# Kernel optimization log

Hardware: AMD Instinct MI355X
Metric: run time of the kernel (lower is better)

## Reference

```python
import jax, jax.numpy as jnp
import numpy as np

B, H, DH = 1, 16, 128
HID, MLP = 2048, 8192
LT, LI = 256, 2048
L = LT + LI


def _layernorm(x, eps=1e-6):
    mu = jnp.mean(x, axis=-1, keepdims=True)
    var = jnp.mean((x - mu) ** 2, axis=-1, keepdims=True)
    return (x - mu) * jax.lax.rsqrt(var + eps)


def _rmsnorm(x, scale, eps=1e-6):
    rr = jax.lax.rsqrt(jnp.mean(x * x, axis=-1, keepdims=True) + eps)
    return x * rr * scale


def _apply_rope(x, pe):
    # x: (B,H,L,D) -> (B,H,L,D/2,1,2); pe: (B,1,L,D/2,2,2)
    xs = x.reshape(*x.shape[:-1], -1, 1, 2)
    out = pe[..., 0] * xs[..., 0] + pe[..., 1] * xs[..., 1]  # (B,H,L,D/2,2)
    return out.reshape(x.shape)


def _qkv_split(x, w, b):
    Bv, Lv, _ = x.shape
    qkv = (x @ w + b).reshape(Bv, Lv, 3, H, DH).transpose(2, 0, 3, 1, 4)  # K B H L D
    return qkv[0], qkv[1], qkv[2]


def setup_inputs() -> dict:
    key = jax.random.key(0)
    ks = jax.random.split(key, 16)
    s = 0.02
    inp = {
        'img': jax.random.normal(ks[0], (B, LI, HID), jnp.float32),
        'txt': jax.random.normal(ks[1], (B, LT, HID), jnp.float32),
        'vec': jax.random.normal(ks[2], (B, HID), jnp.float32),
        'img_mod_w': s * jax.random.normal(ks[3], (HID, 6 * HID), jnp.float32),
        'img_mod_b': jnp.zeros((6 * HID,), jnp.float32),
        'txt_mod_w': s * jax.random.normal(ks[4], (HID, 6 * HID), jnp.float32),
        'txt_mod_b': jnp.zeros((6 * HID,), jnp.float32),
        'img_qkv_w': s * jax.random.normal(ks[5], (HID, 3 * HID), jnp.float32),
        'img_qkv_b': jnp.zeros((3 * HID,), jnp.float32),
        'img_q_scale': jnp.ones((DH,), jnp.float32),
        'img_k_scale': jnp.ones((DH,), jnp.float32),
        'txt_qkv_w': s * jax.random.normal(ks[6], (HID, 3 * HID), jnp.float32),
        'txt_qkv_b': jnp.zeros((3 * HID,), jnp.float32),
        'txt_q_scale': jnp.ones((DH,), jnp.float32),
        'txt_k_scale': jnp.ones((DH,), jnp.float32),
        'img_proj_w': s * jax.random.normal(ks[7], (HID, HID), jnp.float32),
        'img_proj_b': jnp.zeros((HID,), jnp.float32),
        'txt_proj_w': s * jax.random.normal(ks[8], (HID, HID), jnp.float32),
        'txt_proj_b': jnp.zeros((HID,), jnp.float32),
        'img_mlp_w1': s * jax.random.normal(ks[9], (HID, MLP), jnp.float32),
        'img_mlp_b1': jnp.zeros((MLP,), jnp.float32),
        'img_mlp_w2': s * jax.random.normal(ks[10], (MLP, HID), jnp.float32),
        'img_mlp_b2': jnp.zeros((HID,), jnp.float32),
        'txt_mlp_w1': s * jax.random.normal(ks[11], (HID, MLP), jnp.float32),
        'txt_mlp_b1': jnp.zeros((MLP,), jnp.float32),
        'txt_mlp_w2': s * jax.random.normal(ks[12], (MLP, HID), jnp.float32),
        'txt_mlp_b2': jnp.zeros((HID,), jnp.float32),
    }
    # Real RoPE rotation matrices [[cos,-sin],[sin,cos]]: (1,1,L,DH/2,2,2)
    pos = jnp.arange(L, dtype=jnp.float32)
    freqs = 1.0 / (10000.0 ** (jnp.arange(DH // 2, dtype=jnp.float32) / (DH // 2)))
    ang = pos[:, None] * freqs[None, :]
    c, sn = jnp.cos(ang), jnp.sin(ang)
    pe = jnp.stack([jnp.stack([c, -sn], -1), jnp.stack([sn, c], -1)], -2)  # (L,DH/2,2,2)
    inp['pe'] = pe[None, None]
    return inp


def reference(img, txt, vec, pe,
              img_mod_w, img_mod_b, txt_mod_w, txt_mod_b,
              img_qkv_w, img_qkv_b, img_q_scale, img_k_scale,
              txt_qkv_w, txt_qkv_b, txt_q_scale, txt_k_scale,
              img_proj_w, img_proj_b, txt_proj_w, txt_proj_b,
              img_mlp_w1, img_mlp_b1, img_mlp_w2, img_mlp_b2,
              txt_mlp_w1, txt_mlp_b1, txt_mlp_w2, txt_mlp_b2):
    # AdaLN modulation: SiLU(vec) @ W -> 6 chunks of (B,1,HID)
    im = jnp.split(jax.nn.silu(vec) @ img_mod_w + img_mod_b, 6, axis=-1)
    i_sh1, i_sc1, i_g1, i_sh2, i_sc2, i_g2 = [m[:, None, :] for m in im]
    tm = jnp.split(jax.nn.silu(vec) @ txt_mod_w + txt_mod_b, 6, axis=-1)
    t_sh1, t_sc1, t_g1, t_sh2, t_sc2, t_g2 = [m[:, None, :] for m in tm]

    img_mod = (1 + i_sc1) * _layernorm(img) + i_sh1
    iq, ik, iv = _qkv_split(img_mod, img_qkv_w, img_qkv_b)
    iq = _rmsnorm(iq, img_q_scale)
    ik = _rmsnorm(ik, img_k_scale)

    txt_mod = (1 + t_sc1) * _layernorm(txt) + t_sh1
    tq, tk, tv = _qkv_split(txt_mod, txt_qkv_w, txt_qkv_b)
    tq = _rmsnorm(tq, txt_q_scale)
    tk = _rmsnorm(tk, txt_k_scale)

    # concat text then image along sequence (B,H,L,D)
    q = jnp.concatenate([tq, iq], axis=2)
    k = jnp.concatenate([tk, ik], axis=2)
    v = jnp.concatenate([tv, iv], axis=2)
    q = _apply_rope(q, pe)
    k = _apply_rope(k, pe)

    scores = jnp.einsum('bhqd,bhkd->bhqk', q, k) / np.float32(np.sqrt(DH))
    a = jax.nn.softmax(scores, axis=-1)
    o = jnp.einsum('bhqk,bhkd->bhqd', a, v)
    attn = o.transpose(0, 2, 1, 3).reshape(o.shape[0], -1, H * DH)  # (B,L,HID)

    txt_a, img_a = attn[:, :LT], attn[:, LT:]

    img = img + i_g1 * (img_a @ img_proj_w + img_proj_b)
    h = (1 + i_sc2) * _layernorm(img) + i_sh2
    h = jax.nn.gelu(h @ img_mlp_w1 + img_mlp_b1, approximate=True)
    img = img + i_g2 * (h @ img_mlp_w2 + img_mlp_b2)

    txt = txt + t_g1 * (txt_a @ txt_proj_w + txt_proj_b)
    h = (1 + t_sc2) * _layernorm(txt) + t_sh2
    h = jax.nn.gelu(h @ txt_mlp_w1 + txt_mlp_b1, approximate=True)
    txt = txt + t_g2 * (h @ txt_mlp_w2 + txt_mlp_b2)

    return img, txt
```

## Files before the change

kernel.cpp:

```cpp
#include <hip/hip_runtime.h>

using u16 = unsigned short;
typedef __bf16 bf16x8 __attribute__((ext_vector_type(8)));
typedef float f32x4 __attribute__((ext_vector_type(4)));

__device__ inline u16 f2bf(float f){
  unsigned u = __float_as_uint(f);
  u += 0x7fff + ((u >> 16) & 1);
  return (u16)(u >> 16);
}

__device__ inline float wredsum(float v){
  #pragma unroll
  for (int o = 32; o; o >>= 1) v += __shfl_xor(v, o, 64);
  return v;
}

__device__ inline void gld16(const u16* g, u16* lds){
  __builtin_amdgcn_global_load_lds(
      (const __attribute__((address_space(1))) unsigned int*)g,
      (__attribute__((address_space(3))) unsigned int*)lds, 16, 0, 0);
}

__global__ void mod_matvec_k(const float* __restrict__ vec,
    const float* __restrict__ wi, const float* __restrict__ bi,
    const float* __restrict__ wt, const float* __restrict__ bt,
    float* __restrict__ oi, float* __restrict__ ot)
{
  __shared__ float sv[2048];
  __shared__ float red[4][64];
  int tid = threadIdx.x;
  for (int i = tid; i < 2048; i += 256){ float v = vec[i]; sv[i] = v / (1.0f + __expf(-v)); }
  __syncthreads();
  int j0 = blockIdx.x * 64;
  bool ist = j0 >= 12288;
  const float* w = ist ? wt : wi;
  const float* b = ist ? bt : bi;
  float* o = ist ? ot : oi;
  int col = (ist ? j0 - 12288 : j0) + (tid & 63);
  int kq = tid >> 6;
  float acc = 0.f;
  const float* wp = w + col;
  for (int k = kq * 512; k < kq * 512 + 512; ++k) acc += sv[k] * wp[(long long)k * 12288];
  red[kq][tid & 63] = acc;
  __syncthreads();
  if (kq == 0){
    o[col] = red[0][tid] + red[1][tid] + red[2][tid] + red[3][tid] + b[col];
  }
}

struct TcArgs {
  const float* in[8];
  u16* out[8];
  int K[8];
  int N[8];
  int base[9];
};

__global__ void tcast8_k(TcArgs a)
{
  __shared__ float tile[32][33];
  int bid = blockIdx.x;
  int w = 0;
  #pragma unroll
  for (int i = 0; i < 8; ++i) if (bid >= a.base[i + 1]) w = i + 1;
  const float* in = a.in[w];
  u16* out = a.out[w];
  int K = a.K[w], N = a.N[w];
  int local = bid - a.base[w];
  int tx = N >> 5;
  int n0 = (local % tx) * 32, k0 = (local / tx) * 32;
  int tid = threadIdx.x;
  int r = tid >> 3, c4 = (tid & 7) * 4;
  float4 v = *(const float4*)&in[(long long)(k0 + r) * N + n0 + c4];
  tile[r][c4 + 0] = v.x; tile[r][c4 + 1] = v.y; tile[r][c4 + 2] = v.z; tile[r][c4 + 3] = v.w;
  __syncthreads();
  int n = tid >> 3, kq = (tid & 7) * 4;
  ushort4 o;
  o.x = f2bf(tile[kq + 0][n]);
  o.y = f2bf(tile[kq + 1][n]);
  o.z = f2bf(tile[kq + 2][n]);
  o.w = f2bf(tile[kq + 3][n]);
  *(ushort4*)&out[(long long)(n0 + n) * K + k0 + kq] = o;
}

__global__ void ln_mod_k(const float* __restrict__ x,
    const float* __restrict__ sh, const float* __restrict__ sc,
    u16* __restrict__ out)
{
  int row = blockIdx.x, tid = threadIdx.x;
  const float* xr = x + (long long)row * 2048;
  float v[8]; float s = 0.f, s2 = 0.f;
  #pragma unroll
  for (int j = 0; j < 8; ++j){ v[j] = xr[tid + j * 256]; s += v[j]; s2 += v[j] * v[j]; }
  s = wredsum(s); s2 = wredsum(s2);
  __shared__ float red[4][2];
  int wave = tid >> 6, lane = tid & 63;
  if (lane == 0){ red[wave][0] = s; red[wave][1] = s2; }
  __syncthreads();
  float S1 = red[0][0] + red[1][0] + red[2][0] + red[3][0];
  float S2 = red[0][1] + red[1][1] + red[2][1] + red[3][1];
  float mu = S1 * (1.0f / 2048.0f);
  float var = S2 * (1.0f / 2048.0f) - mu * mu;
  float rs = rsqrtf(var + 1e-6f);
  u16* orow = out + (long long)row * 2048;
  #pragma unroll
  for (int j = 0; j < 8; ++j){
    int c = tid + j * 256;
    orow[c] = f2bf((1.0f + sc[c]) * (v[j] - mu) * rs + sh[c]);
  }
}

__global__ void qkv_post_k(const float* __restrict__ qkv, int pos0,
    const float* __restrict__ qs, const float* __restrict__ ks,
    const float* __restrict__ pe,
    u16* __restrict__ Q, u16* __restrict__ Ko, u16* __restrict__ Vt)
{
  __shared__ u16 vs[128][72];
  int h = blockIdx.y;
  int t0 = blockIdx.x * 64;
  int tid = threadIdx.x, wave = tid >> 6, lane = tid & 63;
  for (int it = 0; it < 16; ++it){
    int tl = it * 4 + wave;
    int t = t0 + tl;
    const float* rp = qkv + (long long)t * 6144 + h * 128;
    float q0 = rp[lane],        q1 = rp[lane + 64];
    float k0 = rp[2048 + lane], k1 = rp[2048 + lane + 64];
    float v0 = rp[4096 + lane], v1 = rp[4096 + lane + 64];
    float qss = wredsum(q0 * q0 + q1 * q1);
    float kss = wredsum(k0 * k0 + k1 * k1);
    float rq = rsqrtf(qss * (1.0f / 128.0f) + 1e-6f) * 0.08838834764831845f;
    float rk = rsqrtf(kss * (1.0f / 128.0f) + 1e-6f);
    float qn0 = q0 * rq * qs[lane], qn1 = q1 * rq * qs[lane + 64];
    float kn0 = k0 * rk * ks[lane], kn1 = k1 * rk * ks[lane + 64];
    int pos = pos0 + t;
    const float* peb = pe + (long long)pos * 256;
    bool odd = lane & 1;
    float4 p0 = *(const float4*)&peb[(lane >> 1) * 4];
    float4 p1 = *(const float4*)&peb[128 + (lane >> 1) * 4];
    float c00 = odd ? p0.z : p0.x, c01 = odd ? p0.w : p0.y;
    float c10 = odd ? p1.z : p1.x, c11 = odd ? p1.w : p1.y;
    float qp0 = __shfl_xor(qn0, 1, 64), qp1 = __shfl_xor(qn1, 1, 64);
    float kp0 = __shfl_xor(kn0, 1, 64), kp1 = __shfl_xor(kn1, 1, 64);
    float qe0 = odd ? qp0 : qn0, qo0 = odd ? qn0 : qp0;
    float qe1 = odd ? qp1 : qn1, qo1 = odd ? qn1 : qp1;
    float ke0 = odd ? kp0 : kn0, ko0 = odd ? kn0 : kp0;
    float ke1 = odd ? kp1 : kn1, ko1 = odd ? kn1 : kp1;
    u16* Qr = Q  + ((long long)h * 2304 + pos) * 128;
    u16* Kr = Ko + ((long long)h * 2304 + pos) * 128;
    Qr[lane]      = f2bf(c00 * qe0 + c01 * qo0);
    Qr[lane + 64] = f2bf(c10 * qe1 + c11 * qo1);
    Kr[lane]      = f2bf(c00 * ke0 + c01 * ko0);
    Kr[lane + 64] = f2bf(c10 * ke1 + c11 * ko1);
    vs[lane][tl]      = f2bf(v0);
    vs[lane + 64][tl] = f2bf(v1);
  }
  __syncthreads();
  int dd = tid >> 1, co = (tid & 1) * 32;
  u16* vr = Vt + ((long long)h * 128 + dd) * 2304 + pos0 + t0 + co;
  #pragma unroll
  for (int u = 0; u < 8; ++u)
    *(ushort4*)(vr + u * 4) = *(const ushort4*)&vs[dd][co + u * 4];
}

__global__ __launch_bounds__(512)
void fattn_k(const u16* __restrict__ Qb, const u16* __restrict__ Kb,
             const u16* __restrict__ Vt, u16* __restrict__ attn)
{
  __shared__ u16 Pl[128 * 128];
  __shared__ u16 Kl[128 * 128];
  __shared__ u16 Vl[2][128 * 128];

  const int tid  = threadIdx.x;
  const int lane = tid & 63;
  const int wave = tid >> 6;
  const int h  = blockIdx.y;
  const int q0 = blockIdx.x * 128;

  const u16* Qg = Qb + ((long long)h * 2304 + q0) * 128;
  const u16* Kg = Kb + (long long)h * 2304 * 128;
  const u16* Vg = Vt + (long long)h * 128 * 2304;

  const int s_r   = wave * 4 + (lane >> 4);
  const int s_oct = lane & 15;
  auto stage = [&](const u16* g, int ldg, u16* lds){
    #pragma unroll
    for (int i = 0; i < 4; ++i){
      int row = i * 32 + s_r;
      gld16(g + (long long)row * ldg + ((s_oct ^ (row & 7)) * 8),
            lds + (i * 32 + wave * 4) * 128);
    }
  };

  stage(Qg, 128, Pl);
  stage(Kg, 128, Kl);
  stage(Vg, 2304, Vl[0]);
  __syncthreads();

  const int frow = lane & 15;
  const int j0   = lane >> 4;
  const int qrow = wave * 16 + frow;
  bf16x8 aq[4];
  #pragma unroll
  for (int s = 0; s < 4; ++s)
    aq[s] = *(const bf16x8*)&Pl[qrow * 128 + (((s * 4 + j0) ^ (qrow & 7)) * 8)];
  __syncthreads();

  float mrun[4], lrun[4];
  #pragma unroll
  for (int j = 0; j < 4; ++j){ mrun[j] = -3.0e38f; lrun[j] = 0.f; }
  f32x4 oacc[8] = {};

  for (int t = 0; t < 18; ++t){
    asm volatile("s_waitcnt vmcnt(0)" ::: "memory");
    __builtin_amdgcn_sched_barrier(0);
    __builtin_amdgcn_s_barrier();
    __builtin_amdgcn_sched_barrier(0);

    f32x4 sacc[8] = {};
    #pragma unroll
    for (int s = 0; s < 4; ++s){
      #pragma unroll
      for (int n = 0; n < 8; ++n){
        int kr = n * 16 + frow;
        bf16x8 bk = *(const bf16x8*)&Kl[kr * 128 + (((s * 4 + j0) ^ (kr & 7)) * 8)];
        sacc[n] = __builtin_amdgcn_mfma_f32_16x16x32_bf16(aq[s], bk, sacc[n], 0, 0, 0);
      }
    }
    __builtin_amdgcn_sched_barrier(0);
    __builtin_amdgcn_s_barrier();
    __builtin_amdgcn_sched_barrier(0);
    if (t + 1 < 18){
      stage(Kg + (long long)(t + 1) * 128 * 128, 128, Kl);
      stage(Vg + (t + 1) * 128, 2304, Vl[(t + 1) & 1]);
    }
    __builtin_amdgcn_sched_barrier(0);

    float mnew[4], scl[4];
    #pragma unroll
    for (int j = 0; j < 4; ++j){
      float v = sacc[0][j];
      #pragma unroll
      for (int n = 1; n < 8; ++n) v = fmaxf(v, sacc[n][j]);
      #pragma unroll
      for (int o = 8; o; o >>= 1) v = fmaxf(v, __shfl_xor(v, o, 64));
      mnew[j] = fmaxf(mrun[j], v);
      scl[j] = __expf(mrun[j] - mnew[j]);
      mrun[j] = mnew[j];
    }
    #pragma unroll
    for (int j = 0; j < 4; ++j){
      const int row = wave * 16 + j0 * 4 + j;
      float rsum = 0.f;
      #pragma unroll
      for (int n = 0; n < 8; ++n){
        float p = __expf(sacc[n][j] - mnew[j]);
        rsum += p;
        int col = n * 16 + frow;
        Pl[row * 128 + (((col >> 3) ^ (row & 7)) << 3) + (col & 7)] = f2bf(p);
      }
      #pragma unroll
      for (int o = 8; o; o >>= 1) rsum += __shfl_xor(rsum, o, 64);
      lrun[j] = lrun[j] * scl[j] + rsum;
      #pragma unroll
      for (int n = 0; n < 8; ++n) oacc[n][j] *= scl[j];
    }
    asm volatile("s_waitcnt lgkmcnt(0)" ::: "memory");
    __builtin_amdgcn_sched_barrier(0);

    const u16* vl = Vl[t & 1];
    #pragma unroll
    for (int s = 0; s < 4; ++s){
      bf16x8 ap = *(const bf16x8*)&Pl[qrow * 128 + (((s * 4 + j0) ^ (qrow & 7)) * 8)];
      #pragma unroll
      for (int n = 0; n < 8; ++n){
        int dr = n * 16 + frow;
        bf16x8 bv = *(const bf16x8*)&vl[dr * 128 + (((s * 4 + j0) ^ (dr & 7)) * 8)];
        oacc[n] = __builtin_amdgcn_mfma_f32_16x16x32_bf16(ap, bv, oacc[n], 0, 0, 0);
      }
    }
    __builtin_amdgcn_sched_barrier(0);
  }

  float inv[4];
  #pragma unroll
  for (int j = 0; j < 4; ++j) inv[j] = 1.0f / lrun[j];
  #pragma unroll
  for (int n = 0; n < 8; ++n){
    int d = n * 16 + frow;
    #pragma unroll
    for (int j = 0; j < 4; ++j){
      int row = wave * 16 + j0 * 4 + j;
      attn[(long long)(q0 + row) * 2048 + h * 128 + d] = f2bf(oacc[n][j] * inv[j]);
    }
  }
}

template<int MODE>
__global__ __launch_bounds__(512)
void gemm8_k(const u16* __restrict__ Ai, const u16* __restrict__ At, int lda,
             const u16* __restrict__ Bi, const u16* __restrict__ Bt, int ldb,
             const float* __restrict__ bias_i, const float* __restrict__ bias_t,
             const float* __restrict__ res_i,  const float* __restrict__ res_t,
             const float* __restrict__ gate_i, const float* __restrict__ gate_t,
             void* __restrict__ Ci, void* __restrict__ Ct, int ldc, int K)
{
  constexpr int BK = 64;
  constexpr int MR = 4, NR = 2;
  constexpr int AI = 2, BI = 2;

  __shared__ u16 As[2][128 * BK];
  __shared__ u16 Bs[2][128 * BK];

  const int tid  = threadIdx.x;
  const int lane = tid & 63;
  const int wave = tid >> 6;
  const int wm = wave >> 2;
  const int wn = wave & 3;

  const int gx = gridDim.x;
  const int nwg = gx * gridDim.y;
  const int n = blockIdx.x + gx * blockIdx.y;
  const int s_id = (n & 7) * (nwg >> 3) + (n >> 3);
  const int bx = s_id % gx;
  const int by = s_id / gx;

  const bool ist = bx >= 16;
  const int rb = ist ? bx - 16 : bx;
  const u16* Ab = (ist ? At : Ai) + (long long)rb * 128 * lda;
  const u16* Bb = (ist ? Bt : Bi) + (long long)by * 128 * ldb;
  const float* bias = ist ? bias_t : bias_i;
  const float* res  = ist ? res_t  : res_i;
  const float* gate = ist ? gate_t : gate_i;
  void* C = ist ? Ct : Ci;

  const int srow = wave * 8 + (lane >> 3);
  const int sgo  = ((lane & 7) ^ ((lane >> 3) & 7)) * 8;
  const u16* agp[AI]; const u16* bgp[BI];
  int alo[AI], blo[BI];
  #pragma unroll
  for (int i = 0; i < AI; ++i){
    agp[i] = Ab + (long long)(i * 64 + srow) * lda + sgo;
    alo[i] = (i * 64 + wave * 8) * BK;
  }
  #pragma unroll
  for (int i = 0; i < BI; ++i){
    bgp[i] = Bb + (long long)(i * 64 + srow) * ldb + sgo;
    blo[i] = (i * 64 + wave * 8) * BK;
  }

  const int arow0 = wm * 64;
  const int frow  = lane & 15;
  const int fx    = lane & 7;
  const int j0    = lane >> 4;

  f32x4 acc[MR][NR] = {};

  #pragma unroll
  for (int i = 0; i < AI; ++i) gld16(agp[i], &As[0][alo[i]]);
  #pragma unroll
  for (int i = 0; i < BI; ++i) gld16(bgp[i], &Bs[0][blo[i]]);
  __builtin_amdgcn_sched_barrier(0);

  const int nt = K / BK;
  for (int t = 0; t < nt; ++t){
    if (t + 1 < nt){
      int k0 = (t + 1) * BK;
      int nb = (t + 1) & 1;
      #pragma unroll
      for (int i = 0; i < AI; ++i) gld16(agp[i] + k0, &As[nb][alo[i]]);
      #pragma unroll
      for (int i = 0; i < BI; ++i) gld16(bgp[i] + k0, &Bs[nb][blo[i]]);
      __builtin_amdgcn_sched_barrier(0);
      asm volatile("s_waitcnt vmcnt(4)" ::: "memory");
    } else {
      asm volatile("s_waitcnt vmcnt(0)" ::: "memory");
    }
    __builtin_amdgcn_sched_barrier(0);
    __builtin_amdgcn_s_barrier();
    __builtin_amdgcn_sched_barrier(0);

    const u16* as = As[t & 1];
    const u16* bs = Bs[t & 1];
    #pragma unroll
    for (int s = 0; s < 2; ++s){
      const int oct = (s * 4 + j0) ^ fx;
      bf16x8 bfr[NR];
      #pragma unroll
      for (int nn = 0; nn < NR; ++nn)
        bfr[nn] = *(const bf16x8*)&bs[(wn * 32 + nn * 16 + frow) * BK + oct * 8];
      __builtin_amdgcn_s_setprio(1);
      #pragma unroll
      for (int m = 0; m < MR; ++m){
        bf16x8 af = *(const bf16x8*)&as[(arow0 + m * 16 + frow) * BK + oct * 8];
        #pragma unroll
        for (int nn = 0; nn < NR; ++nn)
          acc[m][nn] = __builtin_amdgcn_mfma_f32_16x16x32_bf16(af, bfr[nn], acc[m][nn], 0, 0, 0);
      }
      __builtin_amdgcn_s_setprio(0);
    }
    __builtin_amdgcn_sched_barrier(0);
    __builtin_amdgcn_s_barrier();
    __builtin_amdgcn_sched_barrier(0);
  }

  const int lr = (lane >> 4) * 4;
  const int lc = lane & 15;
  const long long rowb = (long long)rb * 128 + arow0;
  const long long colb = (long long)by * 128 + wn * 32;
  #pragma unroll
  for (int mi = 0; mi < MR; ++mi){
    #pragma unroll
    for (int ni = 0; ni < NR; ++ni){
      long long col = colb + ni * 16 + lc;
      float bv = bias ? bias[col] : 0.0f;
      #pragma unroll
      for (int j = 0; j < 4; ++j){
        long long row = rowb + mi * 16 + lr + j;
        float v = acc[mi][ni][j] + bv;
        long long ci = row * (long long)ldc + col;
        if constexpr (MODE == 0) ((float*)C)[ci] = v;
        else if constexpr (MODE == 2) ((float*)C)[ci] = res[ci] + gate[col] * v;
        else {
          float z2 = 1.5957691216057308f * (v + 0.044715f * v * v * v);
          ((u16*)C)[ci] = f2bf(v / (1.0f + __expf(-z2)));
        }
      }
    }
  }
}

extern "C" void kernel_launch(void* const* d_in, const int* in_sizes, int n_in,
                              void* d_out, int out_size, void* d_ws, size_t ws_size,
                              hipStream_t stream)
{
  const float* img        = (const float*)d_in[0];
  const float* txt        = (const float*)d_in[1];
  const float* vec        = (const float*)d_in[2];
  const float* img_mod_w  = (const float*)d_in[3];
  const float* img_mod_b  = (const float*)d_in[4];
  const float* txt_mod_w  = (const float*)d_in[5];
  const float* txt_mod_b  = (const float*)d_in[6];
  const float* img_qkv_w  = (const float*)d_in[7];
  const float* img_qkv_b  = (const float*)d_in[8];
  const float* img_q_s    = (const float*)d_in[9];
  const float* img_k_s    = (const float*)d_in[10];
  const float* txt_qkv_w  = (const float*)d_in[11];
  const float* txt_qkv_b  = (const float*)d_in[12];
  const float* txt_q_s    = (const float*)d_in[13];
  const float* txt_k_s    = (const float*)d_in[14];
  const float* img_proj_w = (const float*)d_in[15];
  const float* img_proj_b = (const float*)d_in[16];
  const float* txt_proj_w = (const float*)d_in[17];
  const float* txt_proj_b = (const float*)d_in[18];
  const float* img_mlp_w1 = (const float*)d_in[19];
  const float* img_mlp_b1 = (const float*)d_in[20];
  const float* img_mlp_w2 = (const float*)d_in[21];
  const float* img_mlp_b2 = (const float*)d_in[22];
  const float* txt_mlp_w1 = (const float*)d_in[23];
  const float* txt_mlp_b1 = (const float*)d_in[24];
  const float* txt_mlp_w2 = (const float*)d_in[25];
  const float* txt_mlp_b2 = (const float*)d_in[26];
  const float* pe         = (const float*)d_in[27];

  char* ws = (char*)d_ws;
  size_t off = 0;
  auto alloc = [&](size_t b){ void* p = ws + off; off = (off + b + 255) & ~(size_t)255; return p; };

  u16* wq_i = (u16*)alloc(6144ll * 2048 * 2);
  u16* wq_t = (u16*)alloc(6144ll * 2048 * 2);
  u16* wp_i = (u16*)alloc(2048ll * 2048 * 2);
  u16* wp_t = (u16*)alloc(2048ll * 2048 * 2);
  u16* w1_i = (u16*)alloc(8192ll * 2048 * 2);
  u16* w1_t = (u16*)alloc(8192ll * 2048 * 2);
  u16* w2_i = (u16*)alloc(2048ll * 8192 * 2);
  u16* w2_t = (u16*)alloc(2048ll * 8192 * 2);
  float* mod_i = (float*)alloc(12288 * 4);
  float* mod_t = (float*)alloc(12288 * 4);
  u16* Qb   = (u16*)alloc(16ll * 2304 * 128 * 2);
  u16* Kb   = (u16*)alloc(16ll * 2304 * 128 * 2);
  u16* Vt   = (u16*)alloc(16ll * 2304 * 128 * 2);
  u16* attn = (u16*)alloc(2304ll * 2048 * 2);
  char* big = (char*)alloc(4ll * 2304 * 2304 * 4);

  u16*   xin_i = (u16*)big;
  u16*   xin_t = (u16*)(big + 8388608);
  float* qkv_i = (float*)(big + 9437184);
  float* qkv_t = (float*)(big + 59768832);
  float* y1_i  = (float*)big;
  float* y1_t  = (float*)(big + 16777216);
  u16*   ln2_i = (u16*)(big + 18874368);
  u16*   ln2_t = (u16*)(big + 27262976);
  u16*   h_i   = (u16*)(big + 28311552);
  u16*   h_t   = (u16*)(big + 61865984);

  mod_matvec_k<<<384, 256, 0, stream>>>(vec, img_mod_w, img_mod_b, txt_mod_w, txt_mod_b, mod_i, mod_t);

  {
    TcArgs a;
    const float* ins[8] = {img_qkv_w, txt_qkv_w, img_proj_w, txt_proj_w,
                           img_mlp_w1, txt_mlp_w1, img_mlp_w2, txt_mlp_w2};
    u16* outs[8] = {wq_i, wq_t, wp_i, wp_t, w1_i, w1_t, w2_i, w2_t};
    int Ks[8] = {2048, 2048, 2048, 2048, 2048, 2048, 8192, 8192};
    int Ns[8] = {6144, 6144, 2048, 2048, 8192, 8192, 2048, 2048};
    int b = 0;
    for (int i = 0; i < 8; ++i){
      a.in[i] = ins[i]; a.out[i] = outs[i]; a.K[i] = Ks[i]; a.N[i] = Ns[i];
      a.base[i] = b;
      b += (Ks[i] >> 5) * (Ns[i] >> 5);
    }
    a.base[8] = b;
    tcast8_k<<<b, 256, 0, stream>>>(a);
  }

  ln_mod_k<<<2048, 256, 0, stream>>>(img, mod_i, mod_i + 2048, xin_i);
  ln_mod_k<<<256,  256, 0, stream>>>(txt, mod_t, mod_t + 2048, xin_t);

  gemm8_k<0><<<dim3(18, 48), 512, 0, stream>>>(xin_i, xin_t, 2048, wq_i, wq_t, 2048,
      img_qkv_b, txt_qkv_b, nullptr, nullptr, nullptr, nullptr, qkv_i, qkv_t, 6144, 2048);

  qkv_post_k<<<dim3(32, 16), 256, 0, stream>>>(qkv_i, 256, img_q_s, img_k_s, pe, Qb, Kb, Vt);
  qkv_post_k<<<dim3(4, 16),  256, 0, stream>>>(qkv_t, 0,   txt_q_s, txt_k_s, pe, Qb, Kb, Vt);

  fattn_k<<<dim3(18, 16), 512, 0, stream>>>(Qb, Kb, Vt, attn);

  gemm8_k<2><<<dim3(18, 16), 512, 0, stream>>>(attn + 256 * 2048, attn, 2048, wp_i, wp_t, 2048,
      img_proj_b, txt_proj_b, img, txt, mod_i + 4096, mod_t + 4096, y1_i, y1_t, 2048, 2048);

  ln_mod_k<<<2048, 256, 0, stream>>>(y1_i, mod_i + 6144, mod_i + 8192, ln2_i);
  ln_mod_k<<<256,  256, 0, stream>>>(y1_t, mod_t + 6144, mod_t + 8192, ln2_t);

  gemm8_k<3><<<dim3(18, 64), 512, 0, stream>>>(ln2_i, ln2_t, 2048, w1_i, w1_t, 2048,
      img_mlp_b1, txt_mlp_b1, nullptr, nullptr, nullptr, nullptr, h_i, h_t, 8192, 2048);

  float* out_img = (float*)d_out;
  float* out_txt = out_img + 2048ll * 2048;
  gemm8_k<2><<<dim3(18, 16), 512, 0, stream>>>(h_i, h_t, 8192, w2_i, w2_t, 8192,
      img_mlp_b2, txt_mlp_b2, y1_i, y1_t, mod_i + 10240, mod_t + 10240, out_img, out_txt, 2048, 8192);
}
```

Baseline: 863.2 us.

## Store QKV in bf16, merge img/txt launches, widen weight transpose tiles

The QKV GEMM now writes bf16 instead of fp32, and the post-processing kernel reads bf16, halving intermediate traffic. The img and txt layernorm and qkv_post launches are merged into single grids to cut launch count and tail effects. The weight transpose-cast kernel switches from 32x32 to 64x64 tiles with more work per thread. Rounding QKV to bf16 before the RMS norm adds some precision loss.

```diff
diff --git a/kernel.cpp b/kernel.cpp
--- a/kernel.cpp
+++ b/kernel.cpp
@@ -9,6 +9,7 @@
   u += 0x7fff + ((u >> 16) & 1);
   return (u16)(u >> 16);
 }
+__device__ inline float bf2f(u16 u){ return __uint_as_float((unsigned)u << 16); }
 
 __device__ inline float wredsum(float v){
   #pragma unroll
@@ -57,9 +58,9 @@
   int base[9];
 };
 
-__global__ void tcast8_k(TcArgs a)
-{
-  __shared__ float tile[32][33];
+__global__ void tcast64_k(TcArgs a)
+{
+  __shared__ float tile[64][65];
   int bid = blockIdx.x;
   int w = 0;
   #pragma unroll
@@ -68,28 +69,43 @@
   u16* out = a.out[w];
   int K = a.K[w], N = a.N[w];
   int local = bid - a.base[w];
-  int tx = N >> 5;
-  int n0 = (local % tx) * 32, k0 = (local / tx) * 32;
+  int tx = N >> 6;
+  int n0 = (local % tx) * 64, k0 = (local / tx) * 64;
   int tid = threadIdx.x;
-  int r = tid >> 3, c4 = (tid & 7) * 4;
-  float4 v = *(const float4*)&in[(long long)(k0 + r) * N + n0 + c4];
-  tile[r][c4 + 0] = v.x; tile[r][c4 + 1] = v.y; tile[r][c4 + 2] = v.z; tile[r][c4 + 3] = v.w;
-  __syncthreads();
-  int n = tid >> 3, kq = (tid & 7) * 4;
-  ushort4 o;
-  o.x = f2bf(tile[kq + 0][n]);
-  o.y = f2bf(tile[kq + 1][n]);
-  o.z = f2bf(tile[kq + 2][n]);
-  o.w = f2bf(tile[kq + 3][n]);
-  *(ushort4*)&out[(long long)(n0 + n) * K + k0 + kq] = o;
-}
-
-__global__ void ln_mod_k(const float* __restrict__ x,
-    const float* __restrict__ sh, const float* __restrict__ sc,
-    u16* __restrict__ out)
+  int r = tid >> 2, c0 = (tid & 3) * 16;
+  const float* ir = &in[(long long)(k0 + r) * N + n0 + c0];
+  #pragma unroll
+  for (int j = 0; j < 4; ++j){
+    float4 v = *(const float4*)&ir[j * 4];
+    tile[r][c0 + j * 4 + 0] = v.x; tile[r][c0 + j * 4 + 1] = v.y;
+    tile[r][c0 + j * 4 + 2] = v.z; tile[r][c0 + j * 4 + 3] = v.w;
+  }
+  __syncthreads();
+  int n = tid >> 2, ks = (tid & 3) * 16;
+  u16* orow = &out[(long long)(n0 + n) * K + k0 + ks];
+  #pragma unroll
+  for (int j = 0; j < 4; ++j){
+    ushort4 o;
+    o.x = f2bf(tile[ks + j * 4 + 0][n]);
+    o.y = f2bf(tile[ks + j * 4 + 1][n]);
+    o.z = f2bf(tile[ks + j * 4 + 2][n]);
+    o.w = f2bf(tile[ks + j * 4 + 3][n]);
+    *(ushort4*)&orow[j * 4] = o;
+  }
+}
+
+__global__ void ln_mod_k(const float* __restrict__ xi, const float* __restrict__ xt,
+    const float* __restrict__ sh_i, const float* __restrict__ sc_i,
+    const float* __restrict__ sh_t, const float* __restrict__ sc_t,
+    u16* __restrict__ oi, u16* __restrict__ ot)
 {
   int row = blockIdx.x, tid = threadIdx.x;
-  const float* xr = x + (long long)row * 2048;
+  bool ist = row >= 2048;
+  int r = ist ? row - 2048 : row;
+  const float* xr = (ist ? xt : xi) + (long long)r * 2048;
+  const float* sh = ist ? sh_t : sh_i;
+  const float* sc = ist ? sc_t : sc_i;
+  u16* orow = (ist ? ot : oi) + (long long)r * 2048;
   float v[8]; float s = 0.f, s2 = 0.f;
   #pragma unroll
   for (int j = 0; j < 8; ++j){ v[j] = xr[tid + j * 256]; s += v[j]; s2 += v[j] * v[j]; }
@@ -103,7 +119,6 @@
   float mu = S1 * (1.0f / 2048.0f);
   float var = S2 * (1.0f / 2048.0f) - mu * mu;
   float rs = rsqrtf(var + 1e-6f);
-  u16* orow = out + (long long)row * 2048;
   #pragma unroll
   for (int j = 0; j < 8; ++j){
     int c = tid + j * 256;
@@ -111,22 +126,28 @@
   }
 }
 
-__global__ void qkv_post_k(const float* __restrict__ qkv, int pos0,
-    const float* __restrict__ qs, const float* __restrict__ ks,
+__global__ void qkv_post_k(const u16* __restrict__ qkv_i, const u16* __restrict__ qkv_t,
+    const float* __restrict__ qs_i, const float* __restrict__ ks_i,
+    const float* __restrict__ qs_t, const float* __restrict__ ks_t,
     const float* __restrict__ pe,
     u16* __restrict__ Q, u16* __restrict__ Ko, u16* __restrict__ Vt)
 {
   __shared__ u16 vs[128][72];
   int h = blockIdx.y;
-  int t0 = blockIdx.x * 64;
+  bool ist = blockIdx.x >= 32;
+  int t0 = (ist ? blockIdx.x - 32 : blockIdx.x) * 64;
+  const u16* qkv = ist ? qkv_t : qkv_i;
+  const float* qs = ist ? qs_t : qs_i;
+  const float* ks = ist ? ks_t : ks_i;
+  int pos0 = ist ? 0 : 256;
   int tid = threadIdx.x, wave = tid >> 6, lane = tid & 63;
   for (int it = 0; it < 16; ++it){
     int tl = it * 4 + wave;
     int t = t0 + tl;
-    const float* rp = qkv + (long long)t * 6144 + h * 128;
-    float q0 = rp[lane],        q1 = rp[lane + 64];
-    float k0 = rp[2048 + lane], k1 = rp[2048 + lane + 64];
-    float v0 = rp[4096 + lane], v1 = rp[4096 + lane + 64];
+    const u16* rp = qkv + (long long)t * 6144 + h * 128;
+    float q0 = bf2f(rp[lane]),        q1 = bf2f(rp[lane + 64]);
+    float k0 = bf2f(rp[2048 + lane]), k1 = bf2f(rp[2048 + lane + 64]);
+    float v0 = bf2f(rp[4096 + lane]), v1 = bf2f(rp[4096 + lane + 64]);
     float qss = wredsum(q0 * q0 + q1 * q1);
     float kss = wredsum(k0 * k0 + k1 * k1);
     float rq = rsqrtf(qss * (1.0f / 128.0f) + 1e-6f) * 0.08838834764831845f;
@@ -420,6 +441,7 @@
         float v = acc[mi][ni][j] + bv;
         long long ci = row * (long long)ldc + col;
         if constexpr (MODE == 0) ((float*)C)[ci] = v;
+        else if constexpr (MODE == 1) ((u16*)C)[ci] = f2bf(v);
         else if constexpr (MODE == 2) ((float*)C)[ci] = res[ci] + gate[col] * v;
         else {
           float z2 = 1.5957691216057308f * (v + 0.044715f * v * v * v);
@@ -485,8 +507,8 @@
 
   u16*   xin_i = (u16*)big;
   u16*   xin_t = (u16*)(big + 8388608);
-  float* qkv_i = (float*)(big + 9437184);
-  float* qkv_t = (float*)(big + 59768832);
+  u16*   qkv_i = (u16*)(big + 9437184);
+  u16*   qkv_t = (u16*)(big + 9437184 + 25165824);
   float* y1_i  = (float*)big;
   float* y1_t  = (float*)(big + 16777216);
   u16*   ln2_i = (u16*)(big + 18874368);
@@ -507,28 +529,26 @@
     for (int i = 0; i < 8; ++i){
       a.in[i] = ins[i]; a.out[i] = outs[i]; a.K[i] = Ks[i]; a.N[i] = Ns[i];
       a.base[i] = b;
-      b += (Ks[i] >> 5) * (Ns[i] >> 5);
+      b += (Ks[i] >> 6) * (Ns[i] >> 6);
     }
     a.base[8] = b;
-    tcast8_k<<<b, 256, 0, stream>>>(a);
-  }
-
-  ln_mod_k<<<2048, 256, 0, stream>>>(img, mod_i, mod_i + 2048, xin_i);
-  ln_mod_k<<<256,  256, 0, stream>>>(txt, mod_t, mod_t + 2048, xin_t);
-
-  gemm8_k<0><<<dim3(18, 48), 512, 0, stream>>>(xin_i, xin_t, 2048, wq_i, wq_t, 2048,
+    tcast64_k<<<b, 256, 0, stream>>>(a);
+  }
+
+  ln_mod_k<<<2304, 256, 0, stream>>>(img, txt, mod_i, mod_i + 2048, mod_t, mod_t + 2048, xin_i, xin_t);
+
+  gemm8_k<1><<<dim3(18, 48), 512, 0, stream>>>(xin_i, xin_t, 2048, wq_i, wq_t, 2048,
       img_qkv_b, txt_qkv_b, nullptr, nullptr, nullptr, nullptr, qkv_i, qkv_t, 6144, 2048);
 
-  qkv_post_k<<<dim3(32, 16), 256, 0, stream>>>(qkv_i, 256, img_q_s, img_k_s, pe, Qb, Kb, Vt);
-  qkv_post_k<<<dim3(4, 16),  256, 0, stream>>>(qkv_t, 0,   txt_q_s, txt_k_s, pe, Qb, Kb, Vt);
+  qkv_post_k<<<dim3(36, 16), 256, 0, stream>>>(qkv_i, qkv_t, img_q_s, img_k_s, txt_q_s, txt_k_s,
+      pe, Qb, Kb, Vt);
 
   fattn_k<<<dim3(18, 16), 512, 0, stream>>>(Qb, Kb, Vt, attn);
 
   gemm8_k<2><<<dim3(18, 16), 512, 0, stream>>>(attn + 256 * 2048, attn, 2048, wp_i, wp_t, 2048,
       img_proj_b, txt_proj_b, img, txt, mod_i + 4096, mod_t + 4096, y1_i, y1_t, 2048, 2048);
 
-  ln_mod_k<<<2048, 256, 0, stream>>>(y1_i, mod_i + 6144, mod_i + 8192, ln2_i);
-  ln_mod_k<<<256,  256, 0, stream>>>(y1_t, mod_t + 6144, mod_t + 8192, ln2_t);
+  ln_mod_k<<<2304, 256, 0, stream>>>(y1_i, y1_t, mod_i + 6144, mod_i + 8192, mod_t + 6144, mod_t + 8192, ln2_i, ln2_t);
 
   gemm8_k<3><<<dim3(18, 64), 512, 0, stream>>>(ln2_i, ln2_t, 2048, w1_i, w1_t, 2048,
       img_mlp_b1, txt_mlp_b1, nullptr, nullptr, nullptr, nullptr, h_i, h_t, 8192, 2048);
```

After: 839.5 us. 2.7% less time.
